# Optimization experiments

Hardware: AMD Instinct MI355X
Metric: run time of the kernel (lower is better)

The kernel has to match this reference:

```python
import jax, jax.numpy as jnp
import numpy as np
from jax import lax

KERNEL = 15
IGNORE = 255


def setup_inputs() -> dict:
    key = jax.random.key(0)
    k1, k2 = jax.random.split(key)
    B, C, H, W = 32, 2, 480, 864
    logits = jax.random.normal(k1, (B, C, H, W), dtype=jnp.float32)
    labels = jax.random.randint(k2, (B, H, W), 0, 2, dtype=jnp.int32)
    return {"logits": logits, "labels": labels}


def _boundary_edgemap(labels):
    # labels: [B, H, W] int32 with values in {0, 1, IGNORE}
    lbl = labels.astype(jnp.int32)
    # np_label = label*255, with ignore pixels set to 0 (matches cv2 path)
    np_label = jnp.where(lbl == IGNORE, 0, lbl * 255)
    win = (1, KERNEL, KERNEL)
    strides = (1, 1, 1)
    # cv2.erode with ones kernel == 15x15 min filter (border value +inf -> pad 255)
    erosion = lax.reduce_window(np_label, jnp.int32(255), lax.min, win, strides, "SAME")
    # cv2.dilate == 15x15 max filter (border value -inf -> pad 0)
    dilation = lax.reduce_window(np_label, jnp.int32(0), lax.max, win, strides, "SAME")
    boundary = dilation - erosion  # >0 exactly on the morphological boundary band
    edgemap = jnp.where(boundary > 0, lbl, IGNORE)
    edgemap = jnp.where(lbl == IGNORE, IGNORE, edgemap)
    return edgemap


def reference(logits, labels):
    # logits: [B, C, H, W] log-probabilities, labels: [B, H, W]
    edgemap = _boundary_edgemap(labels)  # [B, H, W]
    valid = edgemap != IGNORE
    tgt = jnp.where(valid, edgemap, 0)  # safe index for ignored pixels
    # gather logits[b, tgt, h, w] -> [B, H, W]
    picked = jnp.take_along_axis(logits, tgt[:, None, :, :], axis=1)[:, 0]
    # NLLLoss with ignore_index: mean of -logp over valid pixels
    n_valid = jnp.maximum(jnp.sum(valid), 1)
    loss = -jnp.sum(jnp.where(valid, picked, 0.0)) / n_valid.astype(logits.dtype)
    return loss
```

## Files before the change

### kernel.cpp

```cpp
#include <hip/hip_runtime.h>


namespace {
constexpr int B_ = 32;
constexpr int H_ = 480;
constexpr int W_ = 864;
constexpr int TW = 64;
constexpr int TH = 32;
constexpr int R_ = 7;
constexpr int LH = TH + 2 * R_;
constexpr int WC = 20;
constexpr int HC = TW / 4;
constexpr int GX = (W_ + TW - 1) / TW;
constexpr int GY = H_ / TH;
constexpr int NBLK = GX * GY * B_;
}

__device__ __forceinline__ unsigned fold4(unsigned x) {
  x |= x >> 16;
  x |= x >> 8;
  return x & 0xFFu;
}

__device__ __forceinline__ unsigned flag_of(int v) {
  return (v == 0 || v == 255) ? 1u : (v == 1 ? 2u : 0u);
}

extern "C" __global__ __launch_bounds__(256, 8)
void boundary_loss_main(const float* __restrict__ logits,
                        const int* __restrict__ labels,
                        double2* __restrict__ partials)
{
  __shared__ unsigned sflag[LH][WC];
  __shared__ unsigned sraw[LH][WC];
  __shared__ unsigned hfl[LH][HC];
  __shared__ double red_s[4];
  __shared__ unsigned red_c[4];

  const int tid = threadIdx.x;
  const int tile_w = blockIdx.x * TW;
  const int tile_h = blockIdx.y * TH;
  const int b = blockIdx.z;

  const int* __restrict__ lab = labels + (size_t)b * H_ * W_;
  const float* __restrict__ lg0 = logits + (size_t)b * 2 * H_ * W_;
  const float* __restrict__ lg1 = lg0 + (size_t)H_ * W_;

  int4 lv[4];
#pragma unroll
  for (int u = 0; u < 4; ++u) {
    const int it = tid + 256 * u;
    const int r = it / WC;
    const int wcc = it - r * WC;
    const int gh = tile_h - R_ + r;
    const int gw = tile_w - 8 + wcc * 4;
    lv[u] = make_int4(200, 200, 200, 200);
    if (it < LH * WC && gh >= 0 && gh < H_ && gw >= 0 && gw < W_)
      lv[u] = *(const int4*)(lab + (size_t)gh * W_ + gw);
  }

  const int r0 = tid >> 4;
  const int wcp = tid & 15;
  const int gw0 = tile_w + wcp * 4;
  const bool inb = gw0 < W_;
  float4 pA0 = make_float4(0, 0, 0, 0), pA1 = pA0, pB0 = pA0, pB1 = pA0;
  if (inb) {
    const size_t offA = (size_t)(tile_h + r0) * W_ + gw0;
    const size_t offB = offA + (size_t)16 * W_;
    pA0 = *(const float4*)(lg0 + offA);
    pA1 = *(const float4*)(lg1 + offA);
    pB0 = *(const float4*)(lg0 + offB);
    pB1 = *(const float4*)(lg1 + offB);
  }

#pragma unroll
  for (int u = 0; u < 4; ++u) {
    const int it = tid + 256 * u;
    if (it < LH * WC) {
      const int r = it / WC;
      const int wcc = it - r * WC;
      const int4 v = lv[u];
      const unsigned raw = (unsigned)(v.x & 0xFF) | ((unsigned)(v.y & 0xFF) << 8) |
                           ((unsigned)(v.z & 0xFF) << 16) | ((unsigned)(v.w & 0xFF) << 24);
      const unsigned flg = flag_of(v.x) | (flag_of(v.y) << 8) |
                           (flag_of(v.z) << 16) | (flag_of(v.w) << 24);
      sraw[r][wcc] = raw;
      sflag[r][wcc] = flg;
    }
  }
  __syncthreads();

  for (int it = tid; it < LH * HC; it += 256) {
    const int r = it >> 4;
    const int wc = it & 15;
    const unsigned w0 = sflag[r][wc];
    const unsigned w1 = sflag[r][wc + 1];
    const unsigned w2 = sflag[r][wc + 2];
    const unsigned w3 = sflag[r][wc + 3];
    const unsigned w4 = sflag[r][wc + 4];
    const unsigned core = fold4(w1 | w2 | w3);
    const unsigned o0 = core | fold4(w0 >> 8);
    const unsigned o1 = core | fold4(w0 >> 16) | (w4 & 0xFFu);
    const unsigned o2 = core | (w0 >> 24) | fold4(w4 & 0xFFFFu);
    const unsigned o3 = core | fold4(w4 & 0xFFFFFFu);
    hfl[r][wc] = o0 | (o1 << 8) | (o2 << 16) | (o3 << 24);
  }
  __syncthreads();

  double lsum = 0.0;
  unsigned lcnt = 0;
  if (inb) {
    unsigned accA = 0, accB = 0;
#pragma unroll
    for (int k = 0; k < 15; ++k) {
      accA |= hfl[r0 + k][wcp];
      accB |= hfl[r0 + 16 + k][wcp];
    }
    const unsigned crawA = sraw[r0 + R_][wcp + 2];
    const unsigned crawB = sraw[r0 + 16 + R_][wcp + 2];
    const float cA0[4] = {pA0.x, pA0.y, pA0.z, pA0.w};
    const float cA1[4] = {pA1.x, pA1.y, pA1.z, pA1.w};
    const float cB0[4] = {pB0.x, pB0.y, pB0.z, pB0.w};
    const float cB1[4] = {pB1.x, pB1.y, pB1.z, pB1.w};
#pragma unroll
    for (int j = 0; j < 4; ++j) {
      const unsigned fA = (accA >> (8 * j)) & 0xFFu;
      const unsigned lA = (crawA >> (8 * j)) & 0xFFu;
      const bool okA = (fA == 3u) && (lA != 255u);
      lsum += okA ? (double)(lA ? cA1[j] : cA0[j]) : 0.0;
      lcnt += okA;
      const unsigned fB = (accB >> (8 * j)) & 0xFFu;
      const unsigned lB = (crawB >> (8 * j)) & 0xFFu;
      const bool okB = (fB == 3u) && (lB != 255u);
      lsum += okB ? (double)(lB ? cB1[j] : cB0[j]) : 0.0;
      lcnt += okB;
    }
  }

#pragma unroll
  for (int off = 32; off > 0; off >>= 1) {
    lsum += __shfl_down(lsum, off, 64);
    lcnt += __shfl_down(lcnt, off, 64);
  }
  const int wave = tid >> 6;
  if ((tid & 63) == 0) { red_s[wave] = lsum; red_c[wave] = lcnt; }
  __syncthreads();
  if (tid == 0) {
    const double s = red_s[0] + red_s[1] + red_s[2] + red_s[3];
    const double c = (double)(red_c[0] + red_c[1] + red_c[2] + red_c[3]);
    const int bid = (blockIdx.z * GY + blockIdx.y) * GX + blockIdx.x;
    partials[bid] = make_double2(s, c);
  }
}

extern "C" __global__ __launch_bounds__(1024)
void boundary_loss_final(const double2* __restrict__ partials,
                         float* __restrict__ out)
{
  __shared__ double red_s[16];
  __shared__ double red_c[16];
  const int tid = threadIdx.x;
  double s = 0.0, c = 0.0;
  for (int i = tid; i < NBLK; i += 1024) {
    const double2 p = partials[i];
    s += p.x;
    c += p.y;
  }
#pragma unroll
  for (int off = 32; off > 0; off >>= 1) {
    s += __shfl_down(s, off, 64);
    c += __shfl_down(c, off, 64);
  }
  const int wave = tid >> 6;
  if ((tid & 63) == 0) { red_s[wave] = s; red_c[wave] = c; }
  __syncthreads();
  if (tid == 0) {
    double ts = 0.0, tc = 0.0;
#pragma unroll
    for (int i = 0; i < 16; ++i) { ts += red_s[i]; tc += red_c[i]; }
    if (tc < 1.0) tc = 1.0;
    out[0] = (float)(-ts / tc);
  }
}

extern "C" void kernel_launch(void* const* d_in, const int* in_sizes, int n_in,
                              void* d_out, int out_size, void* d_ws, size_t ws_size,
                              hipStream_t stream)
{
  const float* logits = (const float*)d_in[0];
  const int* labels = (const int*)d_in[1];
  float* out = (float*)d_out;
  double2* partials = (double2*)d_ws;

  dim3 grid(GX, GY, B_);
  boundary_loss_main<<<grid, 256, 0, stream>>>(logits, labels, partials);
  boundary_loss_final<<<1, 1024, 0, stream>>>(partials, out);
}
```

Before: 193.3 us.

## Load logits via direct global-to-LDS loads and fold raw labels into flags

```diff
diff --git a/kernel.cpp b/kernel.cpp
--- a/kernel.cpp
+++ b/kernel.cpp
@@ -16,6 +16,9 @@
 constexpr int NBLK = GX * GY * B_;
 }
 
+typedef const __attribute__((address_space(1))) void GVOID;
+typedef __attribute__((address_space(3))) void LVOID;
+
 __device__ __forceinline__ unsigned fold4(unsigned x) {
   x |= x >> 16;
   x |= x >> 8;
@@ -23,7 +26,7 @@
 }
 
 __device__ __forceinline__ unsigned flag_of(int v) {
-  return (v == 0 || v == 255) ? 1u : (v == 1 ? 2u : 0u);
+  return (v == 0) ? 1u : (v == 1) ? 2u : (v == 255) ? 5u : 0u;
 }
 
 extern "C" __global__ __launch_bounds__(256, 8)
@@ -31,8 +34,8 @@
                         const int* __restrict__ labels,
                         double2* __restrict__ partials)
 {
+  __shared__ float slg[2][TH][TW];
   __shared__ unsigned sflag[LH][WC];
-  __shared__ unsigned sraw[LH][WC];
   __shared__ unsigned hfl[LH][HC];
   __shared__ double red_s[4];
   __shared__ unsigned red_c[4];
@@ -44,7 +47,6 @@
 
   const int* __restrict__ lab = labels + (size_t)b * H_ * W_;
   const float* __restrict__ lg0 = logits + (size_t)b * 2 * H_ * W_;
-  const float* __restrict__ lg1 = lg0 + (size_t)H_ * W_;
 
   int4 lv[4];
 #pragma unroll
@@ -59,18 +61,22 @@
       lv[u] = *(const int4*)(lab + (size_t)gh * W_ + gw);
   }
 
-  const int r0 = tid >> 4;
-  const int wcp = tid & 15;
-  const int gw0 = tile_w + wcp * 4;
-  const bool inb = gw0 < W_;
-  float4 pA0 = make_float4(0, 0, 0, 0), pA1 = pA0, pB0 = pA0, pB1 = pA0;
-  if (inb) {
-    const size_t offA = (size_t)(tile_h + r0) * W_ + gw0;
-    const size_t offB = offA + (size_t)16 * W_;
-    pA0 = *(const float4*)(lg0 + offA);
-    pA1 = *(const float4*)(lg1 + offA);
-    pB0 = *(const float4*)(lg0 + offB);
-    pB1 = *(const float4*)(lg1 + offB);
+  {
+    const int lane = tid & 63;
+    const int wave = tid >> 6;
+    const int lr = lane >> 4;
+    int gcol = tile_w + (lane & 15) * 4;
+    if (gcol > W_ - 4) gcol = W_ - 4;
+#pragma unroll
+    for (int i = 0; i < 4; ++i) {
+      const int chunk = wave * 4 + i;
+      const int ch = chunk >> 3;
+      const int rb = (chunk & 7) * 4;
+      const float* src = lg0 + (size_t)ch * H_ * W_ +
+                         (size_t)(tile_h + rb + lr) * W_ + gcol;
+      __builtin_amdgcn_global_load_lds((GVOID*)src, (LVOID*)&slg[ch][rb][0],
+                                       16, 0, 0);
+    }
   }
 
 #pragma unroll
@@ -80,11 +86,8 @@
       const int r = it / WC;
       const int wcc = it - r * WC;
       const int4 v = lv[u];
-      const unsigned raw = (unsigned)(v.x & 0xFF) | ((unsigned)(v.y & 0xFF) << 8) |
-                           ((unsigned)(v.z & 0xFF) << 16) | ((unsigned)(v.w & 0xFF) << 24);
       const unsigned flg = flag_of(v.x) | (flag_of(v.y) << 8) |
                            (flag_of(v.z) << 16) | (flag_of(v.w) << 24);
-      sraw[r][wcc] = raw;
       sflag[r][wcc] = flg;
     }
   }
@@ -109,30 +112,36 @@
 
   double lsum = 0.0;
   unsigned lcnt = 0;
-  if (inb) {
+  const int r0 = tid >> 4;
+  const int wcp = tid & 15;
+  if (tile_w + wcp * 4 < W_) {
     unsigned accA = 0, accB = 0;
 #pragma unroll
     for (int k = 0; k < 15; ++k) {
       accA |= hfl[r0 + k][wcp];
       accB |= hfl[r0 + 16 + k][wcp];
     }
-    const unsigned crawA = sraw[r0 + R_][wcp + 2];
-    const unsigned crawB = sraw[r0 + 16 + R_][wcp + 2];
-    const float cA0[4] = {pA0.x, pA0.y, pA0.z, pA0.w};
-    const float cA1[4] = {pA1.x, pA1.y, pA1.z, pA1.w};
-    const float cB0[4] = {pB0.x, pB0.y, pB0.z, pB0.w};
-    const float cB1[4] = {pB1.x, pB1.y, pB1.z, pB1.w};
+    const unsigned cfA = sflag[r0 + R_][wcp + 2];
+    const unsigned cfB = sflag[r0 + 16 + R_][wcp + 2];
+    const float4 a0 = *(const float4*)&slg[0][r0][wcp * 4];
+    const float4 a1 = *(const float4*)&slg[1][r0][wcp * 4];
+    const float4 b0 = *(const float4*)&slg[0][r0 + 16][wcp * 4];
+    const float4 b1 = *(const float4*)&slg[1][r0 + 16][wcp * 4];
+    const float cA0[4] = {a0.x, a0.y, a0.z, a0.w};
+    const float cA1[4] = {a1.x, a1.y, a1.z, a1.w};
+    const float cB0[4] = {b0.x, b0.y, b0.z, b0.w};
+    const float cB1[4] = {b1.x, b1.y, b1.z, b1.w};
 #pragma unroll
     for (int j = 0; j < 4; ++j) {
       const unsigned fA = (accA >> (8 * j)) & 0xFFu;
-      const unsigned lA = (crawA >> (8 * j)) & 0xFFu;
-      const bool okA = (fA == 3u) && (lA != 255u);
-      lsum += okA ? (double)(lA ? cA1[j] : cA0[j]) : 0.0;
+      const unsigned cA = (cfA >> (8 * j)) & 0xFFu;
+      const bool okA = ((fA & 3u) == 3u) && !(cA & 4u);
+      lsum += okA ? (double)((cA & 2u) ? cA1[j] : cA0[j]) : 0.0;
       lcnt += okA;
       const unsigned fB = (accB >> (8 * j)) & 0xFFu;
-      const unsigned lB = (crawB >> (8 * j)) & 0xFFu;
-      const bool okB = (fB == 3u) && (lB != 255u);
-      lsum += okB ? (double)(lB ? cB1[j] : cB0[j]) : 0.0;
+      const unsigned cB = (cfB >> (8 * j)) & 0xFFu;
+      const bool okB = ((fB & 3u) == 3u) && !(cB & 4u);
+      lsum += okB ? (double)((cB & 2u) ? cB1[j] : cB0[j]) : 0.0;
       lcnt += okB;
     }
   }
```

Measured after the change: 195.2 us. Within noise of the previous version (+1.0%).

## Replace shared-memory tiles with per-wave column strips and shuffle-based window OR

Applied to the files above, without the earlier changes.

```diff
diff --git a/kernel.cpp b/kernel.cpp
--- a/kernel.cpp
+++ b/kernel.cpp
@@ -5,135 +5,92 @@
 constexpr int B_ = 32;
 constexpr int H_ = 480;
 constexpr int W_ = 864;
-constexpr int TW = 64;
-constexpr int TH = 32;
+constexpr int HW = H_ * W_;
 constexpr int R_ = 7;
-constexpr int LH = TH + 2 * R_;
-constexpr int WC = 20;
-constexpr int HC = TW / 4;
-constexpr int GX = (W_ + TW - 1) / TW;
-constexpr int GY = H_ / TH;
-constexpr int NBLK = GX * GY * B_;
+constexpr int OC = 50;
+constexpr int TH_ = 32;
+constexpr int LH = TH_ + 2 * R_;
+constexpr int NSX = (W_ + OC - 1) / OC;
+constexpr int NSY = H_ / TH_;
+constexpr int NTILE = B_ * NSY * NSX;
+constexpr int WPB = 4;
+constexpr int NBLKP = NTILE / WPB;
 }
 
-__device__ __forceinline__ unsigned fold4(unsigned x) {
-  x |= x >> 16;
-  x |= x >> 8;
-  return x & 0xFFu;
+__device__ __forceinline__ unsigned hwin15(unsigned x) {
+  unsigned a = x | __shfl_down(x, 1, 64);
+  a |= __shfl_down(a, 2, 64);
+  a |= __shfl_down(a, 4, 64);
+  a |= __shfl_down(a, 7, 64);
+  return __shfl_up(a, 7, 64);
 }
 
-__device__ __forceinline__ unsigned flag_of(int v) {
-  return (v == 0 || v == 255) ? 1u : (v == 1 ? 2u : 0u);
-}
-
-extern "C" __global__ __launch_bounds__(256, 8)
+extern "C" __global__ __launch_bounds__(256, 6)
 void boundary_loss_main(const float* __restrict__ logits,
                         const int* __restrict__ labels,
                         double2* __restrict__ partials)
 {
-  __shared__ unsigned sflag[LH][WC];
-  __shared__ unsigned sraw[LH][WC];
-  __shared__ unsigned hfl[LH][HC];
-  __shared__ double red_s[4];
-  __shared__ unsigned red_c[4];
+  __shared__ double red_s[WPB];
+  __shared__ unsigned red_c[WPB];
 
   const int tid = threadIdx.x;
-  const int tile_w = blockIdx.x * TW;
-  const int tile_h = blockIdx.y * TH;
-  const int b = blockIdx.z;
+  const int lane = tid & 63;
+  const int wv = tid >> 6;
+  const int t = blockIdx.x * WPB + wv;
+  const int b  = t / (NSY * NSX);
+  const int rr = t - b * (NSY * NSX);
+  const int sy = rr / NSX;
+  const int sx = rr - sy * NSX;
 
-  const int* __restrict__ lab = labels + (size_t)b * H_ * W_;
-  const float* __restrict__ lg0 = logits + (size_t)b * 2 * H_ * W_;
-  const float* __restrict__ lg1 = lg0 + (size_t)H_ * W_;
+  const int gr0 = sy * TH_;
+  const int col = sx * OC - R_ + lane;
+  const bool colok = (col >= 0) && (col < W_);
+  const int colc = col < 0 ? 0 : (col >= W_ ? W_ - 1 : col);
 
-  int4 lv[4];
+  const int* __restrict__ lab = labels + b * HW;
+  const float* __restrict__ lg = logits + (size_t)(2 * b) * HW;
+
+  unsigned f0 = 0, f1 = 0, f2 = 0, c0 = 0, c1 = 0, c2 = 0;
 #pragma unroll
-  for (int u = 0; u < 4; ++u) {
-    const int it = tid + 256 * u;
-    const int r = it / WC;
-    const int wcc = it - r * WC;
-    const int gh = tile_h - R_ + r;
-    const int gw = tile_w - 8 + wcc * 4;
-    lv[u] = make_int4(200, 200, 200, 200);
-    if (it < LH * WC && gh >= 0 && gh < H_ && gw >= 0 && gw < W_)
-      lv[u] = *(const int4*)(lab + (size_t)gh * W_ + gw);
+  for (int a = 0; a < LH; ++a) {
+    const int gr = gr0 - R_ + a;
+    const int grc = gr < 0 ? 0 : (gr >= H_ ? H_ - 1 : gr);
+    const int v = lab[grc * W_ + colc];
+    unsigned f = (unsigned)((v == 0) | (v == 255)) | ((unsigned)(v == 1) << 1);
+    const unsigned c = (unsigned)(v == 1) | ((unsigned)(v == 255) << 1);
+    if (gr < 0 || gr >= H_) f = 0;
+    const int sh = 2 * (a & 15);
+    if (a < 16)      { f0 |= f << sh; c0 |= c << sh; }
+    else if (a < 32) { f1 |= f << sh; c1 |= c << sh; }
+    else             { f2 |= f << sh; c2 |= c << sh; }
   }
+  if (!colok) { f0 = f1 = f2 = 0; }
 
-  const int r0 = tid >> 4;
-  const int wcp = tid & 15;
-  const int gw0 = tile_w + wcp * 4;
-  const bool inb = gw0 < W_;
-  float4 pA0 = make_float4(0, 0, 0, 0), pA1 = pA0, pB0 = pA0, pB1 = pA0;
-  if (inb) {
-    const size_t offA = (size_t)(tile_h + r0) * W_ + gw0;
-    const size_t offB = offA + (size_t)16 * W_;
-    pA0 = *(const float4*)(lg0 + offA);
-    pA1 = *(const float4*)(lg1 + offA);
-    pB0 = *(const float4*)(lg0 + offB);
-    pB1 = *(const float4*)(lg1 + offB);
-  }
+  const unsigned h0 = hwin15(f0);
+  const unsigned h1 = hwin15(f1);
+  const unsigned h2 = hwin15(f2);
 
-#pragma unroll
-  for (int u = 0; u < 4; ++u) {
-    const int it = tid + 256 * u;
-    if (it < LH * WC) {
-      const int r = it / WC;
-      const int wcc = it - r * WC;
-      const int4 v = lv[u];
-      const unsigned raw = (unsigned)(v.x & 0xFF) | ((unsigned)(v.y & 0xFF) << 8) |
-                           ((unsigned)(v.z & 0xFF) << 16) | ((unsigned)(v.w & 0xFF) << 24);
-      const unsigned flg = flag_of(v.x) | (flag_of(v.y) << 8) |
-                           (flag_of(v.z) << 16) | (flag_of(v.w) << 24);
-      sraw[r][wcc] = raw;
-      sflag[r][wcc] = flg;
-    }
-  }
-  __syncthreads();
-
-  for (int it = tid; it < LH * HC; it += 256) {
-    const int r = it >> 4;
-    const int wc = it & 15;
-    const unsigned w0 = sflag[r][wc];
-    const unsigned w1 = sflag[r][wc + 1];
-    const unsigned w2 = sflag[r][wc + 2];
-    const unsigned w3 = sflag[r][wc + 3];
-    const unsigned w4 = sflag[r][wc + 4];
-    const unsigned core = fold4(w1 | w2 | w3);
-    const unsigned o0 = core | fold4(w0 >> 8);
-    const unsigned o1 = core | fold4(w0 >> 16) | (w4 & 0xFFu);
-    const unsigned o2 = core | (w0 >> 24) | fold4(w4 & 0xFFFFu);
-    const unsigned o3 = core | fold4(w4 & 0xFFFFFFu);
-    hfl[r][wc] = o0 | (o1 << 8) | (o2 << 16) | (o3 << 24);
-  }
-  __syncthreads();
+  unsigned long long A  = (unsigned long long)h0 | ((unsigned long long)h1 << 32);
+  unsigned long long Bv = (unsigned long long)h1 | ((unsigned long long)h2 << 32);
+  A  |= A  >> 2;  A  |= A  >> 4;  A  |= A  >> 8;  A  |= A  >> 14;
+  Bv |= Bv >> 2;  Bv |= Bv >> 4;  Bv |= Bv >> 8;  Bv |= Bv >> 14;
 
   double lsum = 0.0;
   unsigned lcnt = 0;
-  if (inb) {
-    unsigned accA = 0, accB = 0;
+  const bool outlane = (lane >= R_) && (lane < R_ + OC) && colok;
+  if (outlane) {
+    int lgoff = gr0 * W_ + colc;
 #pragma unroll
-    for (int k = 0; k < 15; ++k) {
-      accA |= hfl[r0 + k][wcp];
-      accB |= hfl[r0 + 16 + k][wcp];
-    }
-    const unsigned crawA = sraw[r0 + R_][wcp + 2];
-    const unsigned crawB = sraw[r0 + 16 + R_][wcp + 2];
-    const float cA0[4] = {pA0.x, pA0.y, pA0.z, pA0.w};
-    const float cA1[4] = {pA1.x, pA1.y, pA1.z, pA1.w};
-    const float cB0[4] = {pB0.x, pB0.y, pB0.z, pB0.w};
-    const float cB1[4] = {pB1.x, pB1.y, pB1.z, pB1.w};
-#pragma unroll
-    for (int j = 0; j < 4; ++j) {
-      const unsigned fA = (accA >> (8 * j)) & 0xFFu;
-      const unsigned lA = (crawA >> (8 * j)) & 0xFFu;
-      const bool okA = (fA == 3u) && (lA != 255u);
-      lsum += okA ? (double)(lA ? cA1[j] : cA0[j]) : 0.0;
-      lcnt += okA;
-      const unsigned fB = (accB >> (8 * j)) & 0xFFu;
-      const unsigned lB = (crawB >> (8 * j)) & 0xFFu;
-      const bool okB = (fB == 3u) && (lB != 255u);
-      lsum += okB ? (double)(lB ? cB1[j] : cB0[j]) : 0.0;
-      lcnt += okB;
+    for (int o = 0; o < TH_; ++o, lgoff += W_) {
+      const unsigned fb = (o < 18) ? ((unsigned)(A >> (2 * o)) & 3u)
+                                   : ((unsigned)(Bv >> (2 * (o - 16))) & 3u);
+      const int ar = o + R_;
+      const unsigned creg = (ar < 16) ? c0 : (ar < 32 ? c1 : c2);
+      const unsigned cb = (creg >> (2 * (ar & 15))) & 3u;
+      const bool ok = (fb == 3u) && ((cb & 2u) == 0u);
+      const float val = lg[lgoff + (int)(cb & 1u) * HW];
+      lsum += ok ? (double)val : 0.0;
+      lcnt += ok ? 1u : 0u;
     }
   }
 
@@ -142,14 +99,12 @@
     lsum += __shfl_down(lsum, off, 64);
     lcnt += __shfl_down(lcnt, off, 64);
   }
-  const int wave = tid >> 6;
-  if ((tid & 63) == 0) { red_s[wave] = lsum; red_c[wave] = lcnt; }
+  if ((tid & 63) == 0) { red_s[wv] = lsum; red_c[wv] = lcnt; }
   __syncthreads();
   if (tid == 0) {
     const double s = red_s[0] + red_s[1] + red_s[2] + red_s[3];
     const double c = (double)(red_c[0] + red_c[1] + red_c[2] + red_c[3]);
-    const int bid = (blockIdx.z * GY + blockIdx.y) * GX + blockIdx.x;
-    partials[bid] = make_double2(s, c);
+    partials[blockIdx.x] = make_double2(s, c);
   }
 }
 
@@ -161,7 +116,7 @@
   __shared__ double red_c[16];
   const int tid = threadIdx.x;
   double s = 0.0, c = 0.0;
-  for (int i = tid; i < NBLK; i += 1024) {
+  for (int i = tid; i < NBLKP; i += 1024) {
     const double2 p = partials[i];
     s += p.x;
     c += p.y;
@@ -192,7 +147,6 @@
   float* out = (float*)d_out;
   double2* partials = (double2*)d_ws;
 
-  dim3 grid(GX, GY, B_);
-  boundary_loss_main<<<grid, 256, 0, stream>>>(logits, labels, partials);
+  boundary_loss_main<<<dim3(NBLKP), 256, 0, stream>>>(logits, labels, partials);
   boundary_loss_final<<<1, 1024, 0, stream>>>(partials, out);
 }
```

Result: no change. 196.2 us (+1.5%).
